# Optimization experiments

Hardware: AMD Instinct MI355X
Metric: run time of the kernel (lower is better)

Reference implementation:

```python
import jax, jax.numpy as jnp
import numpy as np

NUM_BANDS = 8
NUM_CHANNELS = 16
KC = NUM_BANDS * NUM_CHANNELS
EMA_KERNEL_LENGTH = 100
DELTA = 0.1
EPS = 1e-06
S_INIT = 0.04


def setup_inputs() -> dict:
    key = jax.random.key(0)
    kx, = jax.random.split(key, 1)
    x = jax.random.normal(kx, (32, NUM_BANDS, NUM_CHANNELS, 8192), dtype=jnp.float32)
    alpha_raw = jnp.zeros((KC,), dtype=jnp.float32)
    log_s = jnp.full((KC,), float(np.log(S_INIT / (1.0 - S_INIT))), dtype=jnp.float32)
    return {"x": x, "alpha_raw": alpha_raw, "log_s": log_s}


def _build_ema_kernel(log_s):
    # (KC, 1, L_full) causal EMA kernel, then caller slices last L taps
    Lf = EMA_KERNEL_LENGTH
    s = jax.nn.sigmoid(log_s)                      # (KC,)
    j = jnp.arange(Lf, dtype=s.dtype)              # (Lf,)
    impulse = s[:, None] * (1.0 - s[:, None]) ** j[None, :]   # (KC, Lf)
    impulse = impulse / (impulse.sum(axis=1, keepdims=True) + 1e-08)
    kernel = impulse[:, ::-1]                      # flip to causal conv kernel
    return kernel[:, None, :]                      # (KC, 1, Lf)


def reference(x, alpha_raw, log_s):
    B, K, C, T = x.shape
    x_flat = x.reshape(B, KC, T)
    alpha = jax.nn.sigmoid(alpha_raw) * 0.5        # (KC,) in (0, 0.5)
    x_mag = jnp.abs(x_flat)
    L = min(EMA_KERNEL_LENGTH, T)
    kernel = _build_ema_kernel(log_s)[:, :, -L:]   # (KC, 1, L)
    x_padded = jnp.pad(x_mag, ((0, 0), (0, 0), (L - 1, 0)))
    # depthwise causal conv: groups = KC
    M = jax.lax.conv_general_dilated(
        x_padded, kernel,
        window_strides=(1,), padding='VALID',
        feature_group_count=KC,
        dimension_numbers=('NCH', 'OIH', 'NCH'))   # (B, KC, T)
    gain = jnp.clip(M, EPS, None) ** alpha[None, :, None] + DELTA
    out_flat = x_flat / gain
    return out_flat.reshape(B, K, C, T)
```

## Files before the change

### kernel.cpp

```cpp
#include <hip/hip_runtime.h>
#include <math.h>


constexpr int T      = 8192;
constexpr int KC_    = 128;
constexpr int BLOCK  = 256;
constexpr int WPB    = BLOCK / 64;
constexpr int CHUNK  = 4;
constexpr int WELE   = 64 * CHUNK;
constexpr int WPR    = T / WELE;
constexpr int NHALO  = 25;
constexpr float EPS_   = 1e-6f;
constexpr float DELTA_ = 0.1f;
constexpr float LOG2E  = 1.4426950408889634f;

typedef float f32x4 __attribute__((ext_vector_type(4)));

__device__ __forceinline__ float fast_sigmoid(float x) {
    const float e = __builtin_amdgcn_exp2f(-x * LOG2E);
    return __builtin_amdgcn_rcpf(1.0f + e);
}

__device__ __forceinline__ float gain_div(float xv, float M, float alpha) {
    const float Mc = fmaxf(M, EPS_);
    const float g  = __builtin_amdgcn_exp2f(alpha * __builtin_amdgcn_logf(Mc)) + DELTA_;
    return xv * __builtin_amdgcn_rcpf(g);
}

__global__ void agc_setup(const float* __restrict__ alpha_raw,
                          const float* __restrict__ log_s,
                          float* __restrict__ tab)
{
    const int kc = threadIdx.x;
    const float s     = fast_sigmoid(log_s[kc]);
    const float alpha = 0.5f * fast_sigmoid(alpha_raw[kc]);
    const float q     = 1.0f - s;
    const float lq    = __builtin_amdgcn_logf(q);
    const float q4    = (q * q) * (q * q);
    const float q8    = q4 * q4;
    const float q100  = __builtin_amdgcn_exp2f(100.0f * lq);
    const float norm  = (1.0f - q100) + 1e-8f;
    const float w0    = s / norm;
    const float c3    = w0 * q100;
    f32x4* t = reinterpret_cast<f32x4*>(tab);
    t[kc * 2]     = f32x4{q, alpha, w0, c3};
    t[kc * 2 + 1] = f32x4{q4, q8, 0.0f, 0.0f};
}

__global__ __launch_bounds__(BLOCK, 8) void agc_kernel(
    const float* __restrict__ x,
    const float* __restrict__ alpha_raw,
    const float* __restrict__ log_s,
    const float* __restrict__ tab,
    float* __restrict__ out)
{
    __shared__ float Pe[WPB][92];

    const int tid  = threadIdx.x;
    const int lane = tid & 63;
    const int wv   = tid >> 6;
    const int gw   = blockIdx.x * WPB + wv;
    const int row  = gw / WPR;
    const int wrow = gw & (WPR - 1);
    const int kc   = row & (KC_ - 1);
    const float* __restrict__ xrow = x + (size_t)row * T;
    float* __restrict__ orow       = out + (size_t)row * T;
    const f32x4* __restrict__ x4   = reinterpret_cast<const f32x4*>(xrow);
    f32x4* __restrict__ o4         = reinterpret_cast<f32x4*>(orow);

    const int i4 = (wrow << 6) + lane;

    const f32x4 v = x4[i4];
    f32x4 hl = {0.0f, 0.0f, 0.0f, 0.0f};
    const bool halo_lane = (lane < NHALO);
    if (halo_lane && wrow != 0)
        hl = x4[i4 - NHALO];

    float q, alpha, w0, c3, q4, q8;
    if (tab != nullptr) {
        const f32x4 c0 = reinterpret_cast<const f32x4*>(tab)[kc * 2];
        const f32x4 c1 = reinterpret_cast<const f32x4*>(tab)[kc * 2 + 1];
        q = c0.x; alpha = c0.y; w0 = c0.z; c3 = c0.w; q4 = c1.x; q8 = c1.y;
    } else {
        const float s  = fast_sigmoid(log_s[kc]);
        alpha = 0.5f * fast_sigmoid(alpha_raw[kc]);
        q = 1.0f - s;
        const float lq   = __builtin_amdgcn_logf(q);
        q4 = (q * q) * (q * q);
        q8 = q4 * q4;
        const float q100 = __builtin_amdgcn_exp2f(100.0f * lq);
        const float norm = (1.0f - q100) + 1e-8f;
        w0 = s / norm;
        c3 = w0 * q100;
    }

    f32x4 pv;
    pv.x = __shfl(v.x, lane - NHALO, 64);
    pv.y = __shfl(v.y, lane - NHALO, 64);
    pv.z = __shfl(v.z, lane - NHALO, 64);
    pv.w = __shfl(v.w, lane - NHALO, 64);
    if (halo_lane) pv = hl;

    const float a0 = fabsf(v.x),  a1 = fabsf(v.y),  a2 = fabsf(v.z),  a3 = fabsf(v.w);
    const float b0 = fabsf(pv.x), b1 = fabsf(pv.y), b2 = fabsf(pv.z), b3 = fabsf(pv.w);

    const float pA = fmaf(q, fmaf(q, fmaf(q, a0, a1), a2), a3);
    const float pB = fmaf(q, fmaf(q, fmaf(q, b0, b1), b2), b3);

    Pe[wv][NHALO + lane] = pA;
    if (halo_lane) Pe[wv][lane] = pB;

    asm volatile("s_waitcnt lgkmcnt(0)" ::: "memory");

    float accE = Pe[wv][lane];
    float accO = Pe[wv][lane + 1];
    #pragma unroll
    for (int j = 2; j <= 24; j += 2) accE = fmaf(accE, q8, Pe[wv][lane + j]);
    #pragma unroll
    for (int j = 3; j <= 23; j += 2) accO = fmaf(accO, q8, Pe[wv][lane + j]);
    float M = w0 * fmaf(q4, accO, accE);

    f32x4 o;
    M = fmaf(q, M, fmaf(w0, a0, -c3 * b0));  o.x = gain_div(v.x, M, alpha);
    M = fmaf(q, M, fmaf(w0, a1, -c3 * b1));  o.y = gain_div(v.y, M, alpha);
    M = fmaf(q, M, fmaf(w0, a2, -c3 * b2));  o.z = gain_div(v.z, M, alpha);
    M = fmaf(q, M, fmaf(w0, a3, -c3 * b3));  o.w = gain_div(v.w, M, alpha);
    __builtin_nontemporal_store(o, &o4[i4]);
}

extern "C" void kernel_launch(void* const* d_in, const int* in_sizes, int n_in,
                              void* d_out, int out_size, void* d_ws, size_t ws_size,
                              hipStream_t stream) {
    const float* x         = (const float*)d_in[0];
    const float* alpha_raw = (const float*)d_in[1];
    const float* log_s     = (const float*)d_in[2];
    float* out             = (float*)d_out;
    const int nrows = in_sizes[0] / T;
    const int nblocks = nrows * (T / WELE) / WPB;

    float* tab = nullptr;
    if (d_ws != nullptr && ws_size >= (size_t)(KC_ * 8 * sizeof(float))) {
        tab = (float*)d_ws;
        agc_setup<<<1, KC_, 0, stream>>>(alpha_raw, log_s, tab);
    }
    agc_kernel<<<nblocks, BLOCK, 0, stream>>>(x, alpha_raw, log_s, tab, out);
}
```

Baseline: 229.3 us.

## Replace LDS sliding-window EMA with DPP wavefront prefix scan

Turns the per-lane 25-tap windowed sum, previously staged through shared memory, into a difference-of-prefix-sums form. A wavefront-wide weighted scan built from DPP row shifts and row broadcasts replaces it, plus a reduced halo term read back with readlane. The shared-memory array, its wait and the cross-lane shuffles go away. In exchange every lane now issues a full 16-byte global load of the previous window, and there are extra exp2 evaluations and scan steps. The cancellation in the prefix-difference form may cost numerical accuracy.

```diff
diff --git a/kernel.cpp b/kernel.cpp
--- a/kernel.cpp
+++ b/kernel.cpp
@@ -6,8 +6,7 @@
 constexpr int KC_    = 128;
 constexpr int BLOCK  = 256;
 constexpr int WPB    = BLOCK / 64;
-constexpr int CHUNK  = 4;
-constexpr int WELE   = 64 * CHUNK;
+constexpr int WELE   = 256;
 constexpr int WPR    = T / WELE;
 constexpr int NHALO  = 25;
 constexpr float EPS_   = 1e-6f;
@@ -15,6 +14,13 @@
 constexpr float LOG2E  = 1.4426950408889634f;
 
 typedef float f32x4 __attribute__((ext_vector_type(4)));
+
+template<int CTRL, int ROWM>
+__device__ __forceinline__ float dpp0(float v) {
+    return __builtin_bit_cast(float,
+        __builtin_amdgcn_update_dpp(0, __builtin_bit_cast(int, v),
+                                    CTRL, ROWM, 0xf, true));
+}
 
 __device__ __forceinline__ float fast_sigmoid(float x) {
     const float e = __builtin_amdgcn_exp2f(-x * LOG2E);
@@ -36,15 +42,15 @@
     const float alpha = 0.5f * fast_sigmoid(alpha_raw[kc]);
     const float q     = 1.0f - s;
     const float lq    = __builtin_amdgcn_logf(q);
-    const float q4    = (q * q) * (q * q);
-    const float q8    = q4 * q4;
+    const float lq4   = 4.0f * lq;
+    const float q4    = __builtin_amdgcn_exp2f(lq4);
     const float q100  = __builtin_amdgcn_exp2f(100.0f * lq);
     const float norm  = (1.0f - q100) + 1e-8f;
     const float w0    = s / norm;
     const float c3    = w0 * q100;
     f32x4* t = reinterpret_cast<f32x4*>(tab);
     t[kc * 2]     = f32x4{q, alpha, w0, c3};
-    t[kc * 2 + 1] = f32x4{q4, q8, 0.0f, 0.0f};
+    t[kc * 2 + 1] = f32x4{q4, q100, lq4, 0.0f};
 }
 
 __global__ __launch_bounds__(BLOCK, 8) void agc_kernel(
@@ -54,8 +60,6 @@
     const float* __restrict__ tab,
     float* __restrict__ out)
 {
-    __shared__ float Pe[WPB][92];
-
     const int tid  = threadIdx.x;
     const int lane = tid & 63;
     const int wv   = tid >> 6;
@@ -71,35 +75,28 @@
     const int i4 = (wrow << 6) + lane;
 
     const f32x4 v = x4[i4];
-    f32x4 hl = {0.0f, 0.0f, 0.0f, 0.0f};
-    const bool halo_lane = (lane < NHALO);
-    if (halo_lane && wrow != 0)
-        hl = x4[i4 - NHALO];
+    f32x4 pv = {0.0f, 0.0f, 0.0f, 0.0f};
+    if (wrow != 0 || lane >= NHALO)
+        pv = x4[i4 - NHALO];
 
-    float q, alpha, w0, c3, q4, q8;
+    float q, alpha, w0, c3, q4, q100, lq4;
     if (tab != nullptr) {
         const f32x4 c0 = reinterpret_cast<const f32x4*>(tab)[kc * 2];
         const f32x4 c1 = reinterpret_cast<const f32x4*>(tab)[kc * 2 + 1];
-        q = c0.x; alpha = c0.y; w0 = c0.z; c3 = c0.w; q4 = c1.x; q8 = c1.y;
+        q = c0.x; alpha = c0.y; w0 = c0.z; c3 = c0.w;
+        q4 = c1.x; q100 = c1.y; lq4 = c1.z;
     } else {
         const float s  = fast_sigmoid(log_s[kc]);
         alpha = 0.5f * fast_sigmoid(alpha_raw[kc]);
         q = 1.0f - s;
-        const float lq   = __builtin_amdgcn_logf(q);
-        q4 = (q * q) * (q * q);
-        q8 = q4 * q4;
-        const float q100 = __builtin_amdgcn_exp2f(100.0f * lq);
+        const float lq = __builtin_amdgcn_logf(q);
+        lq4  = 4.0f * lq;
+        q4   = __builtin_amdgcn_exp2f(lq4);
+        q100 = __builtin_amdgcn_exp2f(100.0f * lq);
         const float norm = (1.0f - q100) + 1e-8f;
         w0 = s / norm;
         c3 = w0 * q100;
     }
-
-    f32x4 pv;
-    pv.x = __shfl(v.x, lane - NHALO, 64);
-    pv.y = __shfl(v.y, lane - NHALO, 64);
-    pv.z = __shfl(v.z, lane - NHALO, 64);
-    pv.w = __shfl(v.w, lane - NHALO, 64);
-    if (halo_lane) pv = hl;
 
     const float a0 = fabsf(v.x),  a1 = fabsf(v.y),  a2 = fabsf(v.z),  a3 = fabsf(v.w);
     const float b0 = fabsf(pv.x), b1 = fabsf(pv.y), b2 = fabsf(pv.z), b3 = fabsf(pv.w);
@@ -107,18 +104,39 @@
     const float pA = fmaf(q, fmaf(q, fmaf(q, a0, a1), a2), a3);
     const float pB = fmaf(q, fmaf(q, fmaf(q, b0, b1), b2), b3);
 
-    Pe[wv][NHALO + lane] = pA;
-    if (halo_lane) Pe[wv][lane] = pB;
+    const float d  = fmaf(-q100, pB, pA);
+    float e        = dpp0<0x111, 0xf>(d);
+    const float dA = dpp0<0x142, 0xa>(d);
+    const float dB = dpp0<0x143, 0xc>(d);
+    if ((lane & 15) == 0 && lane != 0)
+        e = (lane == 32) ? dB : dA;
 
-    asm volatile("s_waitcnt lgkmcnt(0)" ::: "memory");
+    const float q4_2 = q4 * q4, q4_4 = q4_2 * q4_2, q4_8 = q4_4 * q4_4;
+    const float lf   = (float)lane;
+    const float l31  = (float)(lane & 31);
+    float Ex = e;
+    Ex = fmaf(q4,   dpp0<0x111, 0xf>(Ex), Ex);
+    Ex = fmaf(q4_2, dpp0<0x112, 0xf>(Ex), Ex);
+    Ex = fmaf(q4_4, dpp0<0x114, 0xf>(Ex), Ex);
+    Ex = fmaf(q4_8, dpp0<0x118, 0xf>(Ex), Ex);
+    const float f15 = __builtin_amdgcn_exp2f(fmaxf(l31 - 15.0f, 0.0f) * lq4);
+    Ex = fmaf(f15, dpp0<0x142, 0xa>(Ex), Ex);
+    const float f31 = __builtin_amdgcn_exp2f(fmaxf(lf - 31.0f, 0.0f) * lq4);
+    Ex = fmaf(f31, dpp0<0x143, 0xc>(Ex), Ex);
 
-    float accE = Pe[wv][lane];
-    float accO = Pe[wv][lane + 1];
-    #pragma unroll
-    for (int j = 2; j <= 24; j += 2) accE = fmaf(accE, q8, Pe[wv][lane + j]);
-    #pragma unroll
-    for (int j = 3; j <= 23; j += 2) accO = fmaf(accO, q8, Pe[wv][lane + j]);
-    float M = w0 * fmaf(q4, accO, accE);
+    const float wt = __builtin_amdgcn_exp2f(fmaxf(24.0f - lf, 0.0f) * lq4);
+    float Hs = (lane < NHALO) ? pB * wt : 0.0f;
+    Hs += dpp0<0x111, 0xf>(Hs);
+    Hs += dpp0<0x112, 0xf>(Hs);
+    Hs += dpp0<0x114, 0xf>(Hs);
+    Hs += dpp0<0x118, 0xf>(Hs);
+    Hs += dpp0<0x142, 0xa>(Hs);
+    Hs += dpp0<0x143, 0xc>(Hs);
+    const float H = __builtin_bit_cast(float,
+        __builtin_amdgcn_readlane(__builtin_bit_cast(int, Hs), 63));
+
+    const float qp = __builtin_amdgcn_exp2f(lf * lq4);
+    float M = w0 * fmaf(qp, H, Ex);
 
     f32x4 o;
     M = fmaf(q, M, fmaf(w0, a0, -c3 * b0));  o.x = gain_div(v.x, M, alpha);
@@ -136,7 +154,7 @@
     const float* log_s     = (const float*)d_in[2];
     float* out             = (float*)d_out;
     const int nrows = in_sizes[0] / T;
-    const int nblocks = nrows * (T / WELE) / WPB;
+    const int nblocks = nrows * WPR / WPB;
 
     float* tab = nullptr;
     if (d_ws != nullptr && ws_size >= (size_t)(KC_ * 8 * sizeof(float))) {
```

Result: no change. 228.8 us (-0.2%).
